# Kernel tuning notes

Measured on AMD Instinct MI355X. Metric: run time of the kernel, lower is better.

## Reference

```python
import jax, jax.numpy as jnp
from jax import lax
import numpy as np

DEPTH = 4
D_MODEL = 192
D_INNER = 384
D_STATE = 16
D_CONV = 4
DT_RANK = 12
STRIDE = 4
NUM_PATCHES = 400
L_SEQ = NUM_PATCHES + 1  # +1 cls token appended at the end
EPS = 1e-5


def _rmsnorm(x, w):
    x = x.astype(jnp.float32)
    return (x * lax.rsqrt(jnp.mean(x * x, axis=-1, keepdims=True) + EPS)) * w


def _mamba(x, in_w, cw, cb, xp_w, dtw, dtb, A_log, Dv, ow):
    # x: [B, L, D_MODEL]
    B = x.shape[0]
    xz = jnp.einsum('bld,ed->ble', x, in_w)            # [B, L, 2*D_INNER]
    u, z = jnp.split(xz, 2, axis=-1)                   # [B, L, D_INNER] each
    # causal depthwise conv over L
    u_t = jnp.transpose(u, (0, 2, 1))                  # [B, D_INNER, L]
    u_pad = jnp.pad(u_t, ((0, 0), (0, 0), (D_CONV - 1, 0)))
    conv = lax.conv_general_dilated(
        u_pad, cw[:, None, :], (1,), 'VALID',
        dimension_numbers=('NCH', 'OIH', 'NCH'),
        feature_group_count=D_INNER)                   # [B, D_INNER, L]
    u = jax.nn.silu(conv + cb[:, None])
    u = jnp.transpose(u, (0, 2, 1))                    # [B, L, D_INNER]
    xdbl = jnp.einsum('bld,ed->ble', u, xp_w)          # [B, L, 44]
    dt, Bm, Cm = jnp.split(xdbl, [DT_RANK, DT_RANK + D_STATE], axis=-1)
    dt = jax.nn.softplus(jnp.einsum('blr,dr->bld', dt, dtw) + dtb)  # [B, L, D_INNER]
    A = -jnp.exp(A_log)                                # [D_INNER, D_STATE]
    dA = jnp.exp(dt[..., None] * A)                    # [B, L, D_INNER, D_STATE]
    dBu = dt[..., None] * Bm[:, :, None, :] * u[..., None]
    h0 = jnp.zeros((B, D_INNER, D_STATE), dtype=dA.dtype)

    def step(h, inp):
        dA_t, dBu_t = inp
        h = dA_t * h + dBu_t
        return h, h

    _, hs = lax.scan(step, h0, (jnp.swapaxes(dA, 0, 1), jnp.swapaxes(dBu, 0, 1)))
    hs = jnp.swapaxes(hs, 0, 1)                        # [B, L, D_INNER, D_STATE]
    y = jnp.einsum('bldn,bln->bld', hs, Cm) + u * Dv
    y = y * jax.nn.silu(z)
    return jnp.einsum('bld,ed->ble', y, ow)            # [B, L, D_MODEL]


def _forward(imgs, patch_w, patch_b, pos_embed, cls_token, norm_w, in_proj_w,
             conv_w, conv_b, xproj_w, dt_w, dt_b, A_log, D_param, out_w,
             normf_w, head_w, head_b):
    B = imgs.shape[0]
    # StrideEmbed: non-overlapping strides of 4 bytes -> linear to embed_dim
    x = imgs.reshape(B, NUM_PATCHES, STRIDE) @ patch_w + patch_b  # [B, 400, 192]
    x = x + pos_embed[:, :-1, :]
    cls = cls_token + pos_embed[:, -1:, :]             # [1, 1, 192]
    x = jnp.concatenate([x, jnp.broadcast_to(cls, (B, 1, D_MODEL))], axis=1)
    hidden = x
    residual = None
    for i in range(DEPTH):
        residual = hidden if residual is None else hidden + residual  # fp32 residual stream
        h = _rmsnorm(residual, norm_w[i])
        hidden = _mamba(h, in_proj_w[i], conv_w[i], conv_b[i], xproj_w[i],
                        dt_w[i], dt_b[i], A_log[i], D_param[i], out_w[i])
    x = _rmsnorm(hidden + residual, normf_w)
    cls_out = x[:, -1, :]                              # [B, 192]
    logits = cls_out @ head_w.T + head_b               # [B, 1000]
    return logits


def setup_inputs() -> dict:
    key = jax.random.key(0)
    ks = jax.random.split(key, 16)
    B = 32
    rn = lambda k, s, sc: jax.random.normal(k, s, dtype=jnp.float32) * sc
    A_log = jnp.broadcast_to(jnp.log(jnp.arange(1.0, D_STATE + 1.0, dtype=jnp.float32)),
                             (DEPTH, D_INNER, D_STATE))
    return {
        'imgs': rn(ks[0], (B, 1, 40, 40), 1.0),
        'patch_w': rn(ks[1], (STRIDE, D_MODEL), 0.1),
        'patch_b': jnp.zeros((D_MODEL,), jnp.float32),
        'pos_embed': rn(ks[2], (1, L_SEQ, D_MODEL), 0.02),
        'cls_token': rn(ks[3], (1, 1, D_MODEL), 0.02),
        'norm_w': jnp.ones((DEPTH, D_MODEL), jnp.float32),
        'in_proj_w': rn(ks[4], (DEPTH, 2 * D_INNER, D_MODEL), 0.05),
        'conv_w': rn(ks[5], (DEPTH, D_INNER, D_CONV), 0.3),
        'conv_b': jnp.zeros((DEPTH, D_INNER), jnp.float32),
        'xproj_w': rn(ks[6], (DEPTH, DT_RANK + 2 * D_STATE, D_INNER), 0.05),
        'dt_w': rn(ks[7], (DEPTH, D_INNER, DT_RANK), 0.1),
        'dt_b': rn(ks[8], (DEPTH, D_INNER), 0.5) - 4.0,
        'A_log': A_log,
        'D_param': jnp.ones((DEPTH, D_INNER), jnp.float32),
        'out_w': rn(ks[9], (DEPTH, D_MODEL, D_INNER), 0.05),
        'normf_w': jnp.ones((D_MODEL,), jnp.float32),
        'head_w': rn(ks[10], (1000, D_MODEL), 0.05),
        'head_b': jnp.zeros((1000,), jnp.float32),
    }


def reference(imgs, patch_w, patch_b, pos_embed, cls_token, norm_w, in_proj_w,
              conv_w, conv_b, xproj_w, dt_w, dt_b, A_log, D_param, out_w,
              normf_w, head_w, head_b):
    return _forward(imgs, patch_w, patch_b, pos_embed, cls_token, norm_w,
                    in_proj_w, conv_w, conv_b, xproj_w, dt_w, dt_b, A_log,
                    D_param, out_w, normf_w, head_w, head_b)
```

## Files before the change

kernel.cpp:

```cpp
#include <hip/hip_runtime.h>
#include <hip/hip_bf16.h>

#define B_SZ 32
#define LSEQ 401
#define NT (B_SZ * LSEQ)
#define DM 192
#define DI 384
#define DS 16
#define EPSF 1e-5f
#define NCH 16

typedef __attribute__((ext_vector_type(8))) short short8;
typedef __attribute__((ext_vector_type(4))) float f32x4;
typedef __hip_bfloat16 bf16;

#define OFF_IMGS    0
#define OFF_PATCHW  51200
#define OFF_PATCHB  51968
#define OFF_POS     52160
#define OFF_CLS     129152
#define OFF_NORMW   129344
#define OFF_INW     130112
#define OFF_CONVW   719936
#define OFF_CONVB   726080
#define OFF_XPROJW  727616
#define OFF_DTW     795200
#define OFF_DTB     813632
#define OFF_ALOG    815168
#define OFF_DP      839744
#define OFF_OUTW    841280
#define OFF_NORMF   1136192
#define OFF_HEADW   1136384
#define OFF_HEADB   1328384
#define OFF_TOTAL   1329384

#define WB_INW   0
#define WB_XPJ   589824
#define WB_OUT   688128
#define WB_DTW   983040
#define WB_TOTAL 1032192

__device__ __forceinline__ int chunk_s(int c) { return c == 0 ? 0 : 25 * c + 1; }
__device__ __forceinline__ int chunk_e(int c) { return 25 * c + 26; }

__device__ __forceinline__ float ldsrc(const void* p, int off, int isbf) {
  return isbf ? __bfloat162float(((const bf16*)p)[off]) : ((const float*)p)[off];
}
__device__ __forceinline__ float fast_silu(float z) {
  return z * __builtin_amdgcn_rcpf(1.f + __expf(-z));
}
__device__ __forceinline__ float fast_softplus(float x) {
  float e = __expf(x);
  return (x > 15.f) ? x : __logf(1.f + e);
}
__device__ __forceinline__ float bfbits(unsigned short u) {
  return __uint_as_float(((unsigned int)u) << 16);
}

#define DPP_ADD(x, ctrl) \
  x += __int_as_float(__builtin_amdgcn_update_dpp(0, __float_as_int(x), ctrl, 0xF, 0xF, true))
__device__ __forceinline__ float row_sum16(float x) {
  DPP_ADD(x, 0xB1);
  DPP_ADD(x, 0x4E);
  DPP_ADD(x, 0x124);
  DPP_ADD(x, 0x128);
  return x;
}

struct P18 { const void* p[18]; };

__global__ __launch_bounds__(256) void k_convwb(P18 t, float* __restrict__ fin,
                                                bf16* __restrict__ wb) {
  static const int st[19] = {OFF_IMGS, OFF_PATCHW, OFF_PATCHB, OFF_POS, OFF_CLS,
                             OFF_NORMW, OFF_INW, OFF_CONVW, OFF_CONVB, OFF_XPROJW,
                             OFF_DTW, OFF_DTB, OFF_ALOG, OFF_DP, OFF_OUTW,
                             OFF_NORMF, OFF_HEADW, OFF_HEADB, OFF_TOTAL};
  int isbf = (((const unsigned short*)t.p[5])[0] == 0x3F80) ? 1 : 0;
  int idx = blockIdx.x * 256 + threadIdx.x;
  if (idx < OFF_TOTAL) {
    int lo = 0;
#pragma unroll
    for (int i = 1; i < 18; ++i) if (idx >= st[i]) lo = i;
    fin[idx] = ldsrc(t.p[lo], idx - st[lo], isbf);
  } else if (idx < OFF_TOTAL + WB_TOTAL) {
    int j = idx - OFF_TOTAL;
    float v;
    if (j < WB_XPJ) {
      v = ldsrc(t.p[6], j, isbf);
    } else if (j < WB_OUT) {
      int i2 = j - WB_XPJ;
      int l = i2 / (64 * 384);
      int r = (i2 / 384) & 63;
      int k = i2 % 384;
      v = (r < 44) ? ldsrc(t.p[9], l * 44 * 384 + r * 384 + k, isbf) : 0.f;
    } else if (j < WB_DTW) {
      v = ldsrc(t.p[14], j - WB_OUT, isbf);
    } else {
      int i2 = j - WB_DTW;
      int l = i2 / (384 * 32);
      int r = i2 % (384 * 32);
      int d = r >> 5;
      int k = r & 31;
      v = (k < 12) ? ldsrc(t.p[10], l * 4608 + d * 12 + k, isbf) : 0.f;
    }
    wb[j] = __float2bfloat16(v);
  }
}

__device__ __forceinline__ void inproj_4w(const bf16 (*shb)[200],
                                          const bf16* __restrict__ Win,
                                          bf16* __restrict__ xb,
                                          bf16* __restrict__ zb,
                                          int row0, int tid) {
  int lane = tid & 63, wave = tid >> 6;
  int q = lane >> 4, mlo = lane & 15;
  short8 afrA[6], afrB[6];
#pragma unroll
  for (int kk = 0; kk < 6; ++kk) {
    afrA[kk] = *(const short8*)&shb[mlo][kk * 32 + q * 8];
    afrB[kk] = *(const short8*)&shb[16 + mlo][kk * 32 + q * 8];
  }
  const bf16* wbase = Win + (size_t)(wave * 192 + mlo) * DM + q * 8;
  bf16* dst = (wave < 2) ? xb : zb;
  int ncol0 = (wave < 2) ? wave * 192 : (wave - 2) * 192;
#pragma unroll
  for (int jh = 0; jh < 4; ++jh) {
    short8 Bb[18];
#pragma unroll
    for (int j = 0; j < 3; ++j)
#pragma unroll
      for (int kk = 0; kk < 6; ++kk)
        Bb[j * 6 + kk] = *(const short8*)(wbase + (size_t)(jh * 3 + j) * 16 * DM + kk * 32);
#pragma unroll
    for (int j = 0; j < 3; ++j) {
      f32x4 aA = {}, aB = {};
#pragma unroll
      for (int kk = 0; kk < 6; ++kk) {
        aA = __builtin_amdgcn_mfma_f32_16x16x32_bf16(afrA[kk], Bb[j * 6 + kk], aA, 0, 0, 0);
        aB = __builtin_amdgcn_mfma_f32_16x16x32_bf16(afrB[kk], Bb[j * 6 + kk], aB, 0, 0, 0);
      }
      int n = ncol0 + (jh * 3 + j) * 16 + mlo;
#pragma unroll
      for (int i = 0; i < 4; ++i) {
        dst[(size_t)(row0 + q * 4 + i) * DI + n] = __float2bfloat16(aA[i]);
        dst[(size_t)(row0 + 16 + q * 4 + i) * DI + n] = __float2bfloat16(aB[i]);
      }
    }
  }
}

__global__ __launch_bounds__(256)
__attribute__((amdgpu_waves_per_eu(2, 2)))
void k_embedin(const float* __restrict__ fin,
               float* __restrict__ residual,
               const bf16* __restrict__ Win,
               bf16* __restrict__ xb,
               bf16* __restrict__ zb) {
  __shared__ bf16 shb[32][200];
  const float* imgs = fin + OFF_IMGS;
  const float* pw   = fin + OFF_PATCHW;
  const float* pb   = fin + OFF_PATCHB;
  const float* pos  = fin + OFF_POS;
  const float* cls  = fin + OFF_CLS;
  const float* nw0  = fin + OFF_NORMW;
  int tid = threadIdx.x;
  int row0 = blockIdx.x * 32;
#pragma unroll
  for (int rr = 0; rr < 2; ++rr) {
    int row = rr * 16 + (tid >> 4), g = tid & 15;
    int t = row0 + row;
    int b = t / LSEQ, l = t % LSEQ;
    float im[4];
    if (l < 400) {
#pragma unroll
      for (int s = 0; s < 4; ++s) im[s] = imgs[b * 1600 + l * 4 + s];
    }
    float rn[12], ss = 0.f;
#pragma unroll
    for (int k = 0; k < 12; ++k) {
      int col = g + 16 * k;
      float v;
      if (l < 400) {
        v = pb[col] + pos[l * DM + col];
#pragma unroll
        for (int s = 0; s < 4; ++s) v = fmaf(im[s], pw[s * DM + col], v);
      } else {
        v = cls[col] + pos[400 * DM + col];
      }
      residual[(size_t)t * DM + col] = v;
      rn[k] = v;
      ss = fmaf(v, v, ss);
    }
    ss = row_sum16(ss);
    float sres = rsqrtf(ss / (float)DM + EPSF);
#pragma unroll
    for (int k = 0; k < 12; ++k) {
      int col = g + 16 * k;
      shb[row][col] = __float2bfloat16(rn[k] * sres * nw0[col]);
    }
  }
  __syncthreads();
  inproj_4w(shb, Win, xb, zb, row0, tid);
}

__global__ __launch_bounds__(512) void k_xdt(const bf16* __restrict__ xb,
                                             const float* __restrict__ cw,
                                             const float* __restrict__ cb,
                                             const bf16* __restrict__ Wbf,
                                             float* __restrict__ xdbl,
                                             const bf16* __restrict__ dtwb,
                                             const float* __restrict__ dtb,
                                             bf16* __restrict__ ub,
                                             bf16* __restrict__ dto) {
  __shared__ bf16  sxt[19][392];
  __shared__ bf16  su[16][392];
  __shared__ float4 scw4[384];
  __shared__ float scb[384];
  __shared__ float sxp[2][16][48];
  __shared__ bf16  sxb[16][32];
  int row0 = blockIdx.x * 16;
  int tid = threadIdx.x;
  for (int i = tid; i < 19 * 48; i += 512) {
    int r = i / 48, c8 = i - r * 48;
    int t = row0 - 3 + r;
    if (t < 0) t = 0;
    *(short8*)&sxt[r][c8 * 8] = *(const short8*)(xb + (size_t)t * DI + c8 * 8);
  }
  for (int i = tid; i < 384; i += 512) {
    scw4[i] = ((const float4*)cw)[i];
    scb[i] = cb[i];
  }
  __syncthreads();
  for (int i = tid; i < 768; i += 512) {
    int tok = i / 48;
    int c8 = i - tok * 48;
    int d0 = c8 * 8;
    int t = row0 + tok;
    int l = t % LSEQ;
    float xr[4][8];
#pragma unroll
    for (int k = 0; k < 4; ++k) {
      short8 v = *(const short8*)&sxt[tok + k][d0];
      bool ok = (l - 3 + k) >= 0;
#pragma unroll
      for (int j = 0; j < 8; ++j) {
        unsigned int uu = ((unsigned int)(unsigned short)v[j]) << 16;
        xr[k][j] = ok ? __uint_as_float(uu) : 0.f;
      }
    }
    short8 uvv;
#pragma unroll
    for (int j = 0; j < 8; ++j) {
      float4 w = scw4[d0 + j];
      float a = scb[d0 + j];
      a = fmaf(xr[0][j], w.x, a);
      a = fmaf(xr[1][j], w.y, a);
      a = fmaf(xr[2][j], w.z, a);
      a = fmaf(xr[3][j], w.w, a);
      bf16 h = __float2bfloat16(fast_silu(a));
      uvv[j] = *reinterpret_cast<short*>(&h);
    }
    *(short8*)&su[tok][d0] = uvv;
    *(short8*)(ub + (size_t)t * DI + d0) = uvv;
  }
  __syncthreads();
  int lane = tid & 63;
  int wave = tid >> 6;
  int q = lane >> 4;
  int mlo = lane & 15;
  if (wave < 6) {
    int colw = (wave % 3) * 16;
    int kh = wave / 3;
    f32x4 acc = {};
    for (int k0 = 0; k0 < 192; k0 += 32) {
      short8 a = *(const short8*)&su[mlo][kh * 192 + k0 + q * 8];
      short8 b = *(const short8*)(Wbf + (size_t)(colw + mlo) * DI + kh * 192 + k0 + q * 8);
      acc = __builtin_amdgcn_mfma_f32_16x16x32_bf16(a, b, acc, 0, 0, 0);
    }
#pragma unroll
    for (int i = 0; i < 4; ++i) sxp[kh][q * 4 + i][colw + mlo] = acc[i];
  }
  __syncthreads();
  for (int i = tid; i < 16 * 44; i += 512) {
    int r = i / 44, c = i - r * 44;
    xdbl[(size_t)(row0 + r) * 44 + c] = sxp[0][r][c] + sxp[1][r][c];
  }
  for (int i = tid; i < 512; i += 512) {
    int tok = i >> 5, k = i & 31;
    sxb[tok][k] = __float2bfloat16(k < 12 ? sxp[0][tok][k] + sxp[1][tok][k] : 0.f);
  }
  __syncthreads();
  short8 afrag = *(const short8*)&sxb[mlo][q * 8];
#pragma unroll
  for (int jt = 0; jt < 3; ++jt) {
    int d = (wave * 3 + jt) * 16 + mlo;
    short8 bfrag = *(const short8*)(dtwb + (size_t)d * 32 + q * 8);
    f32x4 acc = {};
    acc = __builtin_amdgcn_mfma_f32_16x16x32_bf16(afrag, bfrag, acc, 0, 0, 0);
    float dtbv = dtb[d];
#pragma unroll
    for (int i = 0; i < 4; ++i)
      dto[(size_t)(row0 + q * 4 + i) * DI + d] =
          __float2bfloat16(fast_softplus(acc[i] + dtbv));
  }
}

__global__ __launch_bounds__(384)
void k_scanA(const bf16* __restrict__ ub,
             const bf16* __restrict__ dtv,
             const float* __restrict__ xdbl,
             const float* __restrict__ A_log,
             float* __restrict__ Pq,
             float* __restrict__ Hq) {
  __shared__ bf16 sdt[26][384], su[26][384];
  __shared__ float sB[26][16];
  int cc = blockIdx.x, b = blockIdx.y;
  int d = threadIdx.x;
  int s = chunk_s(cc), tc = chunk_e(cc) - s;
  int base = b * LSEQ;
  int ng = tc * 48;
#pragma unroll
  for (int j = 0; j < 4; ++j) {
    int i = d + j * 384;
    if (i < ng) {
      int r = i / 48, c8 = i - r * 48;
      size_t g = (size_t)(base + s + r) * DI + c8 * 8;
      *(short8*)&sdt[r][c8 * 8] = *(const short8*)(dtv + g);
      *(short8*)&su[r][c8 * 8]  = *(const short8*)(ub + g);
    }
  }
  for (int i = d; i < tc * 16; i += 384) {
    int t = i >> 4, col = i & 15;
    sB[t][col] = xdbl[(size_t)(base + s + t) * 44 + 12 + col];
  }
  __syncthreads();
  float A[16], h[16];
#pragma unroll
  for (int j = 0; j < 4; ++j) {
    f32x4 al = *(const f32x4*)&A_log[d * DS + j * 4];
#pragma unroll
    for (int i = 0; i < 4; ++i) { A[j * 4 + i] = -__expf(al[i]); h[j * 4 + i] = 0.f; }
  }
  float S = 0.f;
  for (int t = 0; t < tc; ++t) {
    float dv = bfbits(*(const unsigned short*)&sdt[t][d]);
    float uv = bfbits(*(const unsigned short*)&su[t][d]);
    float w = dv * uv;
    S += dv;
    f32x4 B0 = *(const f32x4*)&sB[t][0];
    f32x4 B1 = *(const f32x4*)&sB[t][4];
    f32x4 B2 = *(const f32x4*)&sB[t][8];
    f32x4 B3 = *(const f32x4*)&sB[t][12];
#pragma unroll
    for (int n = 0; n < 16; ++n) {
      float Bn = (n < 4) ? B0[n] : (n < 8) ? B1[n - 4] : (n < 12) ? B2[n - 8] : B3[n - 12];
      float E = __expf(dv * A[n]);
      h[n] = fmaf(E, h[n], w * Bn);
    }
  }
  size_t si = (((size_t)cc * B_SZ + b) * 384 + d) * 16;
#pragma unroll
  for (int j = 0; j < 4; ++j) {
    f32x4 hv, pv;
#pragma unroll
    for (int i = 0; i < 4; ++i) {
      hv[i] = h[j * 4 + i];
      pv[i] = __expf(A[j * 4 + i] * S);
    }
    *(f32x4*)&Hq[si + j * 4] = hv;
    *(f32x4*)&Pq[si + j * 4] = pv;
  }
}

__global__ __launch_bounds__(256) void k_scanP(const float* __restrict__ Pq,
                                               float* __restrict__ Hq) {
  int idx = blockIdx.x * 256 + threadIdx.x;
  int n = idx & 15;
  int dd = (idx >> 4) % 384;
  int b = idx / (384 * 16);
  float hs = 0.f;
  for (int c = 0; c < NCH - 1; ++c) {
    size_t hi = ((((size_t)c * B_SZ + b) * 384 + dd) * 16) + n;
    float P = Pq[hi];
    float he = Hq[hi];
    hs = fmaf(P, hs, he);
    Hq[hi] = hs;
  }
}

__global__ __launch_bounds__(384)
void k_scanB(const bf16* __restrict__ zb,
             const bf16* __restrict__ ub,
             const bf16* __restrict__ dtv,
             const float* __restrict__ xdbl,
             const float* __restrict__ A_log,
             const float* __restrict__ Dp,
             const float* __restrict__ Hq,
             bf16* __restrict__ yb) {
  __shared__ bf16 sdt[26][384], su[26][384], sz[26][384];
  __shared__ float sB[26][16], sC[26][16];
  int cc = blockIdx.x, b = blockIdx.y;
  int d = threadIdx.x;
  int s = chunk_s(cc), tc = chunk_e(cc) - s;
  int base = b * LSEQ;
  int ng = tc * 48;
#pragma unroll
  for (int j = 0; j < 4; ++j) {
    int i = d + j * 384;
    if (i < ng) {
      int r = i / 48, c8 = i - r * 48;
      size_t g = (size_t)(base + s + r) * DI + c8 * 8;
      *(short8*)&sdt[r][c8 * 8] = *(const short8*)(dtv + g);
      *(short8*)&su[r][c8 * 8]  = *(const short8*)(ub + g);
      *(short8*)&sz[r][c8 * 8]  = *(const short8*)(zb + g);
    }
  }
  for (int i = d; i < tc * 32; i += 384) {
    int t = i >> 5, col = i & 31;
    float v = xdbl[(size_t)(base + s + t) * 44 + 12 + col];
    if (col < 16) sB[t][col] = v;
    else          sC[t][col - 16] = v;
  }
  __syncthreads();
  float A[16], h[16];
#pragma unroll
  for (int j = 0; j < 4; ++j) {
    f32x4 al = *(const f32x4*)&A_log[d * DS + j * 4];
#pragma unroll
    for (int i = 0; i < 4; ++i) { A[j * 4 + i] = -__expf(al[i]); h[j * 4 + i] = 0.f; }
  }
  if (cc > 0) {
    size_t hi = (((size_t)(cc - 1) * B_SZ + b) * 384 + d) * 16;
#pragma unroll
    for (int j = 0; j < 4; ++j) {
      f32x4 hv = *(const f32x4*)&Hq[hi + j * 4];
#pragma unroll
      for (int i = 0; i < 4; ++i) h[j * 4 + i] = hv[i];
    }
  }
  float Dv = Dp[d];
  bf16* py = yb + (size_t)(base + s) * DI + d;
  for (int t = 0; t < tc; ++t) {
    float dv = bfbits(*(const unsigned short*)&sdt[t][d]);
    float uv = bfbits(*(const unsigned short*)&su[t][d]);
    float zv = bfbits(*(const unsigned short*)&sz[t][d]);
    float w = dv * uv;
    f32x4 B0 = *(const f32x4*)&sB[t][0];
    f32x4 B1 = *(const f32x4*)&sB[t][4];
    f32x4 B2 = *(const f32x4*)&sB[t][8];
    f32x4 B3 = *(const f32x4*)&sB[t][12];
    f32x4 C0 = *(const f32x4*)&sC[t][0];
    f32x4 C1 = *(const f32x4*)&sC[t][4];
    f32x4 C2 = *(const f32x4*)&sC[t][8];
    f32x4 C3 = *(const f32x4*)&sC[t][12];
    float y0 = 0.f, y1 = 0.f;
#pragma unroll
    for (int n = 0; n < 16; ++n) {
      float Bn = (n < 4) ? B0[n] : (n < 8) ? B1[n - 4] : (n < 12) ? B2[n - 8] : B3[n - 12];
      float Cn = (n < 4) ? C0[n] : (n < 8) ? C1[n - 4] : (n < 12) ? C2[n - 8] : C3[n - 12];
      float E = __expf(dv * A[n]);
      h[n] = fmaf(E, h[n], w * Bn);
      if (n & 1) y1 = fmaf(h[n], Cn, y1);
      else       y0 = fmaf(h[n], Cn, y0);
    }
    float yv = (y0 + y1 + uv * Dv) * fast_silu(zv);
    py[(size_t)t * DI] = __float2bfloat16(yv);
  }
}

__global__ __launch_bounds__(256)
__attribute__((amdgpu_waves_per_eu(2, 2)))
void k_outin(const bf16* __restrict__ yb,
             const bf16* __restrict__ Wout,
             float* __restrict__ residual,
             const float* __restrict__ nw,
             const bf16* __restrict__ Win,
             bf16* __restrict__ xb,
             bf16* __restrict__ zb) {
  __shared__ bf16  syt[32][392];
  __shared__ float sCt[32][200];
  __shared__ bf16  shb[32][200];
  int tid = threadIdx.x;
  int lane = tid & 63;
  int wave = tid >> 6;
  int row0 = blockIdx.x * 32;
  int q = lane >> 4;
  int mlo = lane & 15;
  {
    const bf16* src = yb + (size_t)row0 * DI;
    short8 v[6];
#pragma unroll
    for (int j = 0; j < 6; ++j) {
      int i = tid + j * 256;
      v[j] = *(const short8*)(src + (i / 48) * DI + (i % 48) * 8);
    }
#pragma unroll
    for (int j = 0; j < 6; ++j) {
      int i = tid + j * 256;
      *(short8*)&syt[i / 48][(i % 48) * 8] = v[j];
    }
  }
  __syncthreads();
  {
    int colw = wave * 48;
    f32x4 acc[2][3] = {};
#pragma unroll
    for (int kh = 0; kh < 2; ++kh) {
      const bf16* brow = Wout + (size_t)(colw + mlo) * DI + kh * 192 + q * 8;
      short8 Bf[18];
#pragma unroll
      for (int j = 0; j < 3; ++j)
#pragma unroll
        for (int k2 = 0; k2 < 6; ++k2)
          Bf[j * 6 + k2] = *(const short8*)(brow + (size_t)j * 16 * DI + k2 * 32);
      short8 afA[6], afB[6];
#pragma unroll
      for (int k2 = 0; k2 < 6; ++k2) {
        afA[k2] = *(const short8*)&syt[mlo][kh * 192 + k2 * 32 + q * 8];
        afB[k2] = *(const short8*)&syt[16 + mlo][kh * 192 + k2 * 32 + q * 8];
      }
#pragma unroll
      for (int k2 = 0; k2 < 6; ++k2) {
#pragma unroll
        for (int j = 0; j < 3; ++j) {
          acc[0][j] = __builtin_amdgcn_mfma_f32_16x16x32_bf16(afA[k2], Bf[j * 6 + k2], acc[0][j], 0, 0, 0);
          acc[1][j] = __builtin_amdgcn_mfma_f32_16x16x32_bf16(afB[k2], Bf[j * 6 + k2], acc[1][j], 0, 0, 0);
        }
      }
    }
#pragma unroll
    for (int rg = 0; rg < 2; ++rg)
#pragma unroll
      for (int j = 0; j < 3; ++j)
#pragma unroll
        for (int i = 0; i < 4; ++i)
          sCt[rg * 16 + q * 4 + i][colw + j * 16 + mlo] = acc[rg][j][i];
  }
  __syncthreads();
#pragma unroll
  for (int rr = 0; rr < 2; ++rr) {
    int row = rr * 16 + (tid >> 4), g = tid & 15;
    int t = row0 + row;
    float* rp = residual + (size_t)t * DM + g * 12;
    float4 r4[3];
#pragma unroll
    for (int j = 0; j < 3; ++j) r4[j] = *(const float4*)(rp + j * 4);
    float rn[12], ss = 0.f;
#pragma unroll
    for (int k = 0; k < 12; ++k) {
      int col = g * 12 + k;
      float x = sCt[row][col] + ((const float*)r4)[k];
      rn[k] = x;
      ss = fmaf(x, x, ss);
    }
    ss = row_sum16(ss);
    float sres = rsqrtf(ss / (float)DM + EPSF);
#pragma unroll
    for (int j = 0; j < 3; ++j) {
      float4 w4;
      w4.x = rn[j * 4 + 0]; w4.y = rn[j * 4 + 1];
      w4.z = rn[j * 4 + 2]; w4.w = rn[j * 4 + 3];
      *(float4*)(rp + j * 4) = w4;
    }
#pragma unroll
    for (int k = 0; k < 12; ++k) {
      int col = g * 12 + k;
      shb[row][col] = __float2bfloat16(rn[k] * sres * nw[col]);
    }
  }
  __syncthreads();
  inproj_4w(shb, Win, xb, zb, row0, tid);
}

__global__ __launch_bounds__(256) void k_lastout(const bf16* __restrict__ yb,
                                                 const bf16* __restrict__ Wout,
                                                 const float* __restrict__ resIn,
                                                 float* __restrict__ clsbuf) {
  __shared__ float sCt[16][200];
  int tid = threadIdx.x;
  int lane = tid & 63;
  int wave = tid >> 6;
  int b0 = blockIdx.x * 16;
  int q = lane >> 4;
  int mlo = lane & 15;
  int colw = wave * 48;
  f32x4 acc[3] = {};
  const bf16* arow = yb + ((size_t)(b0 + mlo) * LSEQ + 400) * DI + q * 8;
  for (int k0 = 0; k0 < DI; k0 += 32) {
    short8 a = *(const short8*)(arow + k0);
#pragma unroll
    for (int j = 0; j < 3; ++j) {
      short8 b = *(const short8*)(Wout + (size_t)(colw + j * 16 + mlo) * DI + k0 + q * 8);
      acc[j] = __builtin_amdgcn_mfma_f32_16x16x32_bf16(a, b, acc[j], 0, 0, 0);
    }
  }
#pragma unroll
  for (int j = 0; j < 3; ++j)
#pragma unroll
    for (int i = 0; i < 4; ++i) sCt[q * 4 + i][colw + j * 16 + mlo] = acc[j][i];
  __syncthreads();
  int row = tid >> 4, g = tid & 15;
  int bb = b0 + row;
#pragma unroll
  for (int k = 0; k < 12; ++k) {
    int col = g + 16 * k;
    clsbuf[(size_t)bb * DM + col] =
        sCt[row][col] + resIn[((size_t)bb * LSEQ + 400) * DM + col];
  }
}

__global__ __launch_bounds__(256) void k_final(const float* __restrict__ clsbuf,
                                               const float* __restrict__ fin,
                                               const void* __restrict__ nw_raw,
                                               void* __restrict__ out) {
  const float* normf  = fin + OFF_NORMF;
  const float* head_w = fin + OFF_HEADW;
  const float* head_b = fin + OFF_HEADB;
  __shared__ float clsv[DM];
  __shared__ float partial[4];
  __shared__ float sres;
  int b = blockIdx.x;
  float r = 0.f;
  if (threadIdx.x < DM) r = clsbuf[(size_t)b * DM + threadIdx.x];
  float ss = r * r;
#pragma unroll
  for (int m = 32; m >= 1; m >>= 1) ss += __shfl_xor(ss, m, 64);
  if ((threadIdx.x & 63) == 0) partial[threadIdx.x >> 6] = ss;
  __syncthreads();
  if (threadIdx.x == 0)
    sres = rsqrtf((partial[0] + partial[1] + partial[2] + partial[3]) / (float)DM + EPSF);
  __syncthreads();
  if (threadIdx.x < DM) clsv[threadIdx.x] = r * sres * normf[threadIdx.x];
  __syncthreads();
  int isbf = (((const unsigned short*)nw_raw)[0] == 0x3F80) ? 1 : 0;
  for (int e = threadIdx.x; e < 1000; e += 256) {
    float acc = head_b[e];
    for (int k = 0; k < DM; ++k) acc = fmaf(clsv[k], head_w[e * DM + k], acc);
    if (isbf) ((bf16*)out)[b * 1000 + e] = __float2bfloat16(acc);
    else      ((float*)out)[b * 1000 + e] = acc;
  }
}

extern "C" void kernel_launch(void* const* d_in, const int* in_sizes, int n_in,
                              void* d_out, int out_size, void* d_ws, size_t ws_size,
                              hipStream_t stream) {
  char* base = (char*)d_ws;
  size_t off = 0;
  auto alloc = [&](size_t bytes) { char* p = base + off; off = (off + bytes + 255) & ~(size_t)255; return p; };
  float* fin      = (float*)alloc((size_t)OFF_TOTAL * 4);
  bf16*  wb       = (bf16*)alloc((size_t)WB_TOTAL * 2);
  float* residual = (float*)alloc((size_t)NT * DM * 4);
  bf16*  xb       = (bf16*)alloc((size_t)NT * DI * 2);
  bf16*  zb       = (bf16*)alloc((size_t)NT * DI * 2);
  bf16*  ub       = (bf16*)alloc((size_t)NT * DI * 2);
  float* xdbl     = (float*)alloc((size_t)NT * 44 * 4);
  bf16*  dtb16    = (bf16*)alloc((size_t)NT * DI * 2);
  float* Pq       = (float*)alloc((size_t)(NCH - 1) * B_SZ * 384 * 16 * 4);
  float* Hq       = (float*)alloc((size_t)(NCH - 1) * B_SZ * 384 * 16 * 4);
  float* clsbuf   = (float*)alloc((size_t)B_SZ * DM * 4);
  bf16*  yb       = ub;

  P18 t;
  for (int i = 0; i < 18; ++i) t.p[i] = d_in[i];
  k_convwb<<<(OFF_TOTAL + WB_TOTAL + 255) / 256, 256, 0, stream>>>(t, fin, wb);

  k_embedin<<<NT / 32, 256, 0, stream>>>(fin, residual, wb + WB_INW, xb, zb);

  for (int layer = 0; layer < 4; ++layer) {
    const float* dtb = fin + OFF_DTB + layer * DI;
    const float* alog = fin + OFF_ALOG + layer * DI * DS;

    k_xdt<<<NT / 16, 512, 0, stream>>>(xb, fin + OFF_CONVW + layer * DI * 4,
                                       fin + OFF_CONVB + layer * DI,
                                       wb + WB_XPJ + layer * 64 * DI, xdbl,
                                       wb + WB_DTW + layer * 384 * 32, dtb, ub, dtb16);

    k_scanA<<<dim3(NCH - 1, B_SZ), 384, 0, stream>>>(ub, dtb16, xdbl, alog, Pq, Hq);
    k_scanP<<<(B_SZ * 384 * 16) / 256, 256, 0, stream>>>(Pq, Hq);
    k_scanB<<<dim3(NCH, B_SZ), 384, 0, stream>>>(zb, ub, dtb16, xdbl, alog,
                                                 fin + OFF_DP + layer * DI, Hq, yb);

    if (layer < 3) {
      k_outin<<<NT / 32, 256, 0, stream>>>(yb, wb + WB_OUT + layer * DM * DI, residual,
                                           fin + OFF_NORMW + (layer + 1) * DM,
                                           wb + WB_INW + (layer + 1) * 768 * DM, xb, zb);
    } else {
      k_lastout<<<2, 256, 0, stream>>>(yb, wb + WB_OUT + 3 * DM * DI, residual, clsbuf);
    }
  }
  k_final<<<B_SZ, 256, 0, stream>>>(clsbuf, fin, d_in[5], d_out);
}
```

Baseline: 551.2 us.

## Fuse conv/x-proj/dt kernel with chunked scan pass A per sequence chunk

Merges the conv+x_proj+dt_proj kernel with the first chunked-scan pass, so each block handles one (chunk, batch) tile of up to 26 tokens and runs the local scan directly from shared memory. This removes one launch per layer and the global re-read of u, dt and B by the scan kernel. The trade-off is a grid that drops from about 800 blocks to 512, larger shared memory per block, and a serial scan that uses only 384 of 512 threads while the remaining waves sit idle, which can reduce parallelism and occupancy.

```diff
diff --git a/kernel.cpp b/kernel.cpp
--- a/kernel.cpp
+++ b/kernel.cpp
@@ -9,6 +9,7 @@
 #define DS 16
 #define EPSF 1e-5f
 #define NCH 16
+#define TCMAX 26
 
 typedef __attribute__((ext_vector_type(8))) short short8;
 typedef __attribute__((ext_vector_type(4))) float f32x4;
@@ -203,40 +204,54 @@
   inproj_4w(shb, Win, xb, zb, row0, tid);
 }
 
-__global__ __launch_bounds__(512) void k_xdt(const bf16* __restrict__ xb,
-                                             const float* __restrict__ cw,
-                                             const float* __restrict__ cb,
-                                             const bf16* __restrict__ Wbf,
-                                             float* __restrict__ xdbl,
-                                             const bf16* __restrict__ dtwb,
-                                             const float* __restrict__ dtb,
-                                             bf16* __restrict__ ub,
-                                             bf16* __restrict__ dto) {
-  __shared__ bf16  sxt[19][392];
-  __shared__ bf16  su[16][392];
-  __shared__ float4 scw4[384];
+__global__ __launch_bounds__(512) void k_xdtA(const bf16* __restrict__ xb,
+                                              const float* __restrict__ cw,
+                                              const float* __restrict__ cb,
+                                              const bf16* __restrict__ Wbf,
+                                              float* __restrict__ xdbl,
+                                              const bf16* __restrict__ dtwb,
+                                              const float* __restrict__ dtb,
+                                              const float* __restrict__ A_log,
+                                              bf16* __restrict__ ub,
+                                              bf16* __restrict__ dto,
+                                              float* __restrict__ Pq,
+                                              float* __restrict__ Hq) {
+  __shared__ __align__(16) bf16  su[32][392];
+  __shared__ __align__(16) char  smemB[22752];
+  __shared__ __align__(16) float4 scw4[384];
   __shared__ float scb[384];
-  __shared__ float sxp[2][16][48];
-  __shared__ bf16  sxb[16][32];
-  int row0 = blockIdx.x * 16;
+  __shared__ __align__(16) float sxp[2][32][48];
+  __shared__ __align__(16) bf16  sxb[32][32];
+  bf16 (*sxt)[392]  = (bf16(*)[392])smemB;
+  bf16 (*sdtl)[384] = (bf16(*)[384])smemB;
+  float (*sB)[16]   = (float(*)[16])(smemB + 19968);
+
+  int cc = blockIdx.x, b = blockIdx.y;
   int tid = threadIdx.x;
-  for (int i = tid; i < 19 * 48; i += 512) {
+  int s = chunk_s(cc), tc = chunk_e(cc) - s;
+  int base = b * LSEQ;
+
+  for (int i = tid; i < (tc + 3) * 48; i += 512) {
     int r = i / 48, c8 = i - r * 48;
-    int t = row0 - 3 + r;
-    if (t < 0) t = 0;
-    *(short8*)&sxt[r][c8 * 8] = *(const short8*)(xb + (size_t)t * DI + c8 * 8);
+    int tt = s - 3 + r;
+    if (tt < 0) tt = 0;
+    *(short8*)&sxt[r][c8 * 8] = *(const short8*)(xb + (size_t)(base + tt) * DI + c8 * 8);
+  }
+  {
+    short8 z = {};
+    for (int i = tid; i < (32 - tc) * 48; i += 512) {
+      int r = tc + i / 48, c8 = i % 48;
+      *(short8*)&su[r][c8 * 8] = z;
+    }
   }
   for (int i = tid; i < 384; i += 512) {
     scw4[i] = ((const float4*)cw)[i];
     scb[i] = cb[i];
   }
   __syncthreads();
-  for (int i = tid; i < 768; i += 512) {
-    int tok = i / 48;
-    int c8 = i - tok * 48;
-    int d0 = c8 * 8;
-    int t = row0 + tok;
-    int l = t % LSEQ;
+  for (int i = tid; i < tc * 48; i += 512) {
+    int tok = i / 48, c8 = i % 48, d0 = c8 * 8;
+    int l = s + tok;
     float xr[4][8];
 #pragma unroll
     for (int k = 0; k < 4; ++k) {
@@ -261,114 +276,95 @@
       uvv[j] = *reinterpret_cast<short*>(&h);
     }
     *(short8*)&su[tok][d0] = uvv;
-    *(short8*)(ub + (size_t)t * DI + d0) = uvv;
-  }
-  __syncthreads();
-  int lane = tid & 63;
-  int wave = tid >> 6;
-  int q = lane >> 4;
-  int mlo = lane & 15;
-  if (wave < 6) {
-    int colw = (wave % 3) * 16;
-    int kh = wave / 3;
+    *(short8*)(ub + (size_t)(base + l) * DI + d0) = uvv;
+  }
+  __syncthreads();
+  int lane = tid & 63, wave = tid >> 6;
+  int q = lane >> 4, mlo = lane & 15;
+  for (int j = wave; j < 12; j += 8) {
+    int rt = j / 6, rem = j % 6, kh = rem / 3, cg = rem % 3;
     f32x4 acc = {};
     for (int k0 = 0; k0 < 192; k0 += 32) {
-      short8 a = *(const short8*)&su[mlo][kh * 192 + k0 + q * 8];
-      short8 b = *(const short8*)(Wbf + (size_t)(colw + mlo) * DI + kh * 192 + k0 + q * 8);
-      acc = __builtin_amdgcn_mfma_f32_16x16x32_bf16(a, b, acc, 0, 0, 0);
-    }
-#pragma unroll
-    for (int i = 0; i < 4; ++i) sxp[kh][q * 4 + i][colw + mlo] = acc[i];
-  }
-  __syncthreads();
-  for (int i = tid; i < 16 * 44; i += 512) {
-    int r = i / 44, c = i - r * 44;
-    xdbl[(size_t)(row0 + r) * 44 + c] = sxp[0][r][c] + sxp[1][r][c];
-  }
-  for (int i = tid; i < 512; i += 512) {
+      short8 a = *(const short8*)&su[rt * 16 + mlo][kh * 192 + k0 + q * 8];
+      short8 bb = *(const short8*)(Wbf + (size_t)(cg * 16 + mlo) * DI + kh * 192 + k0 + q * 8);
+      acc = __builtin_amdgcn_mfma_f32_16x16x32_bf16(a, bb, acc, 0, 0, 0);
+    }
+#pragma unroll
+    for (int i = 0; i < 4; ++i) sxp[kh][rt * 16 + q * 4 + i][cg * 16 + mlo] = acc[i];
+  }
+  __syncthreads();
+  for (int i = tid; i < tc * 44; i += 512) {
+    int r = i / 44, c = i % 44;
+    xdbl[(size_t)(base + s + r) * 44 + c] = sxp[0][r][c] + sxp[1][r][c];
+  }
+  for (int i = tid; i < tc * 16; i += 512) {
+    int t = i >> 4, col = i & 15;
+    sB[t][col] = sxp[0][t][12 + col] + sxp[1][t][12 + col];
+  }
+  for (int i = tid; i < 1024; i += 512) {
     int tok = i >> 5, k = i & 31;
-    sxb[tok][k] = __float2bfloat16(k < 12 ? sxp[0][tok][k] + sxp[1][tok][k] : 0.f);
-  }
-  __syncthreads();
-  short8 afrag = *(const short8*)&sxb[mlo][q * 8];
-#pragma unroll
-  for (int jt = 0; jt < 3; ++jt) {
-    int d = (wave * 3 + jt) * 16 + mlo;
+    sxb[tok][k] = __float2bfloat16((k < 12 && tok < tc) ? sxp[0][tok][k] + sxp[1][tok][k] : 0.f);
+  }
+  __syncthreads();
+#pragma unroll
+  for (int jt = 0; jt < 6; ++jt) {
+    int job = wave + jt * 8;
+    int rt = job / 24, nt = job % 24;
+    int d = nt * 16 + mlo;
+    short8 afrag = *(const short8*)&sxb[rt * 16 + mlo][q * 8];
     short8 bfrag = *(const short8*)(dtwb + (size_t)d * 32 + q * 8);
     f32x4 acc = {};
     acc = __builtin_amdgcn_mfma_f32_16x16x32_bf16(afrag, bfrag, acc, 0, 0, 0);
     float dtbv = dtb[d];
 #pragma unroll
-    for (int i = 0; i < 4; ++i)
-      dto[(size_t)(row0 + q * 4 + i) * DI + d] =
-          __float2bfloat16(fast_softplus(acc[i] + dtbv));
-  }
-}
-
-__global__ __launch_bounds__(384)
-void k_scanA(const bf16* __restrict__ ub,
-             const bf16* __restrict__ dtv,
-             const float* __restrict__ xdbl,
-             const float* __restrict__ A_log,
-             float* __restrict__ Pq,
-             float* __restrict__ Hq) {
-  __shared__ bf16 sdt[26][384], su[26][384];
-  __shared__ float sB[26][16];
-  int cc = blockIdx.x, b = blockIdx.y;
-  int d = threadIdx.x;
-  int s = chunk_s(cc), tc = chunk_e(cc) - s;
-  int base = b * LSEQ;
-  int ng = tc * 48;
-#pragma unroll
-  for (int j = 0; j < 4; ++j) {
-    int i = d + j * 384;
-    if (i < ng) {
-      int r = i / 48, c8 = i - r * 48;
-      size_t g = (size_t)(base + s + r) * DI + c8 * 8;
-      *(short8*)&sdt[r][c8 * 8] = *(const short8*)(dtv + g);
-      *(short8*)&su[r][c8 * 8]  = *(const short8*)(ub + g);
-    }
-  }
-  for (int i = d; i < tc * 16; i += 384) {
-    int t = i >> 4, col = i & 15;
-    sB[t][col] = xdbl[(size_t)(base + s + t) * 44 + 12 + col];
-  }
-  __syncthreads();
-  float A[16], h[16];
-#pragma unroll
-  for (int j = 0; j < 4; ++j) {
-    f32x4 al = *(const f32x4*)&A_log[d * DS + j * 4];
-#pragma unroll
-    for (int i = 0; i < 4; ++i) { A[j * 4 + i] = -__expf(al[i]); h[j * 4 + i] = 0.f; }
-  }
-  float S = 0.f;
-  for (int t = 0; t < tc; ++t) {
-    float dv = bfbits(*(const unsigned short*)&sdt[t][d]);
-    float uv = bfbits(*(const unsigned short*)&su[t][d]);
-    float w = dv * uv;
-    S += dv;
-    f32x4 B0 = *(const f32x4*)&sB[t][0];
-    f32x4 B1 = *(const f32x4*)&sB[t][4];
-    f32x4 B2 = *(const f32x4*)&sB[t][8];
-    f32x4 B3 = *(const f32x4*)&sB[t][12];
-#pragma unroll
-    for (int n = 0; n < 16; ++n) {
-      float Bn = (n < 4) ? B0[n] : (n < 8) ? B1[n - 4] : (n < 12) ? B2[n - 8] : B3[n - 12];
-      float E = __expf(dv * A[n]);
-      h[n] = fmaf(E, h[n], w * Bn);
-    }
-  }
-  size_t si = (((size_t)cc * B_SZ + b) * 384 + d) * 16;
-#pragma unroll
-  for (int j = 0; j < 4; ++j) {
-    f32x4 hv, pv;
-#pragma unroll
     for (int i = 0; i < 4; ++i) {
-      hv[i] = h[j * 4 + i];
-      pv[i] = __expf(A[j * 4 + i] * S);
-    }
-    *(f32x4*)&Hq[si + j * 4] = hv;
-    *(f32x4*)&Pq[si + j * 4] = pv;
+      int row = rt * 16 + q * 4 + i;
+      if (row < tc) {
+        bf16 hv = __float2bfloat16(fast_softplus(acc[i] + dtbv));
+        dto[(size_t)(base + s + row) * DI + d] = hv;
+        sdtl[row][d] = hv;
+      }
+    }
+  }
+  __syncthreads();
+  if (cc < NCH - 1 && tid < 384) {
+    int d = tid;
+    float A[16], h[16];
+#pragma unroll
+    for (int j = 0; j < 4; ++j) {
+      f32x4 al = *(const f32x4*)&A_log[d * DS + j * 4];
+#pragma unroll
+      for (int i = 0; i < 4; ++i) { A[j * 4 + i] = -__expf(al[i]); h[j * 4 + i] = 0.f; }
+    }
+    float S = 0.f;
+    for (int t = 0; t < tc; ++t) {
+      float dv = bfbits(*(const unsigned short*)&sdtl[t][d]);
+      float uv = bfbits(*(const unsigned short*)&su[t][d]);
+      float w = dv * uv;
+      S += dv;
+      f32x4 B0 = *(const f32x4*)&sB[t][0];
+      f32x4 B1 = *(const f32x4*)&sB[t][4];
+      f32x4 B2 = *(const f32x4*)&sB[t][8];
+      f32x4 B3 = *(const f32x4*)&sB[t][12];
+#pragma unroll
+      for (int n = 0; n < 16; ++n) {
+        float Bn = (n < 4) ? B0[n] : (n < 8) ? B1[n - 4] : (n < 12) ? B2[n - 8] : B3[n - 12];
+        float E = __expf(dv * A[n]);
+        h[n] = fmaf(E, h[n], w * Bn);
+      }
+    }
+    size_t si = (((size_t)cc * B_SZ + b) * 384 + d) * 16;
+#pragma unroll
+    for (int j = 0; j < 4; ++j) {
+      f32x4 hv, pv;
+#pragma unroll
+      for (int i = 0; i < 4; ++i) {
+        hv[i] = h[j * 4 + i];
+        pv[i] = __expf(A[j * 4 + i] * S);
+      }
+      *(f32x4*)&Hq[si + j * 4] = hv;
+      *(f32x4*)&Pq[si + j * 4] = pv;
+    }
   }
 }
 
@@ -397,8 +393,8 @@
              const float* __restrict__ Dp,
              const float* __restrict__ Hq,
              bf16* __restrict__ yb) {
-  __shared__ bf16 sdt[26][384], su[26][384], sz[26][384];
-  __shared__ float sB[26][16], sC[26][16];
+  __shared__ bf16 sdt[TCMAX][384], su[TCMAX][384], sz[TCMAX][384];
+  __shared__ float sB[TCMAX][16], sC[TCMAX][16];
   int cc = blockIdx.x, b = blockIdx.y;
   int d = threadIdx.x;
   int s = chunk_s(cc), tc = chunk_e(cc) - s;
@@ -670,12 +666,12 @@
     const float* dtb = fin + OFF_DTB + layer * DI;
     const float* alog = fin + OFF_ALOG + layer * DI * DS;
 
-    k_xdt<<<NT / 16, 512, 0, stream>>>(xb, fin + OFF_CONVW + layer * DI * 4,
-                                       fin + OFF_CONVB + layer * DI,
-                                       wb + WB_XPJ + layer * 64 * DI, xdbl,
-                                       wb + WB_DTW + layer * 384 * 32, dtb, ub, dtb16);
-
-    k_scanA<<<dim3(NCH - 1, B_SZ), 384, 0, stream>>>(ub, dtb16, xdbl, alog, Pq, Hq);
+    k_xdtA<<<dim3(NCH, B_SZ), 512, 0, stream>>>(xb, fin + OFF_CONVW + layer * DI * 4,
+                                                fin + OFF_CONVB + layer * DI,
+                                                wb + WB_XPJ + layer * 64 * DI, xdbl,
+                                                wb + WB_DTW + layer * 384 * 32, dtb,
+                                                alog, ub, dtb16, Pq, Hq);
+
     k_scanP<<<(B_SZ * 384 * 16) / 256, 256, 0, stream>>>(Pq, Hq);
     k_scanB<<<dim3(NCH, B_SZ), 384, 0, stream>>>(zb, ub, dtb16, xdbl, alog,
                                                  fin + OFF_DP + layer * DI, Hq, yb);
```

Result: faster. 533.2 us (-3.3%).
